# Kernel optimization log

Hardware: AMD Instinct MI355X
Metric: run time of the kernel (lower is better)

The kernel has to match this reference:

```python
import jax, jax.numpy as jnp
import numpy as np

# ViT-B on the Lorentz hyperboloid (curvature C): points x = [x_time, x_space],
# x_time = sqrt(||x_space||^2 + C). All linear/conv/norm ops act on the space
# part and recompute time; residuals/attention-midpoints renormalize the full
# Lorentz vector back onto the hyperboloid.
B, IMG, P, CIN, D, H, L = 32, 224, 16, 3, 768, 12, 12
HD = D // H          # per-head space dim (64)
DFF = 2048           # swiglu hidden: int(2/3 * 4*768) aligned to 64
C = 1.0
EPS = 1e-6


def _time(xs):
    return jnp.sqrt(jnp.clip(jnp.sum(xs * xs, -1, keepdims=True) + C, EPS, None))


def _to_lorentz(xs):
    return jnp.concatenate([_time(xs), xs], -1)


def _project(z):
    # renormalize full Lorentz vector so <z,z>_L = -C
    zz = jnp.sum(z[..., 1:] ** 2, -1, keepdims=True) - z[..., :1] ** 2
    return z * (jnp.sqrt(C) / jnp.sqrt(jnp.clip(-zz, EPS, None)))


def _lorentz_ln(x, g, b):
    xs = x[..., 1:]
    mu = xs.mean(-1, keepdims=True)
    var = ((xs - mu) ** 2).mean(-1, keepdims=True)
    xs = (xs - mu) / jnp.sqrt(var + 1e-6) * g + b
    return _to_lorentz(xs)


def _lresnet(x, y, w):
    # Lorentzian weighted residual: midpoint of x and w*y, projected to manifold
    return _project(x + w * y)


def _rope_tables():
    # 2D axial rope over the 14x14 patch grid, identity rotation for 1 cls token
    n = IMG // P
    d4 = HD // 4
    inv = 1.0 / (100.0 ** (np.arange(d4) / d4))
    ang = np.arange(n)[:, None] * inv[None, :]            # [n, d4]
    ay = np.repeat(ang[:, None, :], n, axis=1)            # row angles
    ax = np.repeat(ang[None, :, :], n, axis=0)            # col angles
    a = np.concatenate([ay, ax], -1).reshape(n * n, HD // 2)
    cos = np.concatenate([np.ones((1, HD // 2)), np.cos(a)], 0)
    sin = np.concatenate([np.zeros((1, HD // 2)), np.sin(a)], 0)
    return jnp.asarray(cos, jnp.float32), jnp.asarray(sin, jnp.float32)


def _apply_rope(x, cos, sin):
    # x: [B,N,H,HD]; rotate consecutive pairs (complex multiply)
    xr = x.reshape(*x.shape[:-1], -1, 2)
    x0, x1 = xr[..., 0], xr[..., 1]
    c = cos[None, :, None, :]
    s = sin[None, :, None, :]
    out = jnp.stack([x0 * c - x1 * s, x0 * s + x1 * c], -1)
    return out.reshape(x.shape)


def _attention(x, Wq, Wk, Wv, Wo, cos, sin, scale):
    b, n, _ = x.shape
    xs = x[..., 1:]
    q = (xs @ Wq).reshape(b, n, H, HD)
    k = (xs @ Wk).reshape(b, n, H, HD)
    v = (xs @ Wv).reshape(b, n, H, HD)
    q = _apply_rope(q, cos, sin)
    k = _apply_rope(k, cos, sin)
    qt = _time(q)[..., 0]   # [B,N,H]
    kt = _time(k)[..., 0]
    # Lorentz inner product <q,k>_L = -q_t k_t + q_s . k_s
    inner = jnp.einsum('bnhd,bmhd->bhnm', q, k) - jnp.einsum('bnh,bmh->bhnm', qt, kt)
    attn = jax.nn.softmax((2.0 * C + 2.0 * inner) / scale, axis=-1)
    vf = jnp.concatenate([_time(v), v], -1)               # [B,M,H,HD+1]
    mid = jnp.einsum('bhnm,bmhe->bnhe', attn, vf)         # Lorentzian midpoint
    mid = _project(mid)
    out_s = mid[..., 1:].reshape(b, n, H * HD) @ Wo       # concat heads + proj
    return _to_lorentz(out_s)


def setup_inputs() -> dict:
    key = jax.random.key(0)
    ks = jax.random.split(key, 12)
    std = 0.02
    nrm = lambda k, shape: jax.random.normal(k, shape, jnp.float32) * std
    return {
        'x': jax.random.normal(ks[0], (B, CIN, IMG, IMG), jnp.float32),
        'cls_s': nrm(ks[1], (D - 1,)),
        'Wp': nrm(ks[2], (P, P, CIN + 1, D - 1)),         # HWIO conv kernel
        'ln1_g': jnp.ones((L, D - 1), jnp.float32),
        'ln1_b': jnp.zeros((L, D - 1), jnp.float32),
        'Wq': nrm(ks[3], (L, D - 1, H * HD)),
        'Wk': nrm(ks[4], (L, D - 1, H * HD)),
        'Wv': nrm(ks[5], (L, D - 1, H * HD)),
        'Wo': nrm(ks[6], (L, H * HD, D - 1)),
        'ln2_g': jnp.ones((L, D - 1), jnp.float32),
        'ln2_b': jnp.zeros((L, D - 1), jnp.float32),
        'W1': nrm(ks[7], (L, D - 1, DFF)),
        'W2': nrm(ks[8], (L, D - 1, DFF)),
        'W3': nrm(ks[9], (L, DFF, D - 1)),
        'wy1': jnp.ones((L,), jnp.float32),
        'wy2': jnp.ones((L,), jnp.float32),
        'lnf_g': jnp.ones((D - 1,), jnp.float32),
        'lnf_b': jnp.zeros((D - 1,), jnp.float32),
    }


def reference(x, cls_s, Wp, ln1_g, ln1_b, Wq, Wk, Wv, Wo, ln2_g, ln2_b,
              W1, W2, W3, wy1, wy2, lnf_g, lnf_b):
    b = x.shape[0]
    xs = jnp.transpose(x, (0, 2, 3, 1))                   # BHWC
    xl = _to_lorentz(xs)                                  # pixel-wise time channel
    feat = jax.lax.conv_general_dilated(
        xl, Wp, (P, P), 'VALID',
        dimension_numbers=('NHWC', 'HWIO', 'NHWC'))       # [B,14,14,D-1]
    tok = _to_lorentz(feat).reshape(b, -1, D)             # [B,196,D]
    cls = jnp.broadcast_to(_to_lorentz(cls_s)[None, None, :], (b, 1, D))
    tok = jnp.concatenate([cls, tok], 1)                  # [B,197,D]
    cos, sin = _rope_tables()
    scale = jnp.sqrt(jnp.asarray(H * HD, jnp.float32))
    for l in range(L):
        xn = _lorentz_ln(tok, ln1_g[l], ln1_b[l])
        a = _attention(xn, Wq[l], Wk[l], Wv[l], Wo[l], cos, sin, scale)
        tok = _lresnet(tok, a, wy1[l])
        xn = _lorentz_ln(tok, ln2_g[l], ln2_b[l])
        hs = xn[..., 1:]
        m = _to_lorentz((jax.nn.silu(hs @ W1[l]) * (hs @ W2[l])) @ W3[l])
        tok = _lresnet(tok, m, wy2[l])
    return _lorentz_ln(tok, lnf_g, lnf_b)
```

## Files before the change

### kernel.cpp

```cpp
#include <hip/hip_runtime.h>
#include <hip/hip_bf16.h>

typedef __attribute__((ext_vector_type(8))) short short8;
typedef __attribute__((ext_vector_type(4))) float f32x4;
typedef _Float16 f16x8 __attribute__((ext_vector_type(8)));

#define NLAYER 12
#define NTOK   6304
#define MPAD   6400
#define CONVM  6272

#define QELE     ((size_t)384*208*64)
#define VELE     ((size_t)384*80*232)

static constexpr size_t AL(size_t x){ return (x + 511) & ~(size_t)511; }
static constexpr size_t B_COS    = 0;
static constexpr size_t B_SIN    = AL(B_COS    + (size_t)197*32*4);
static constexpr size_t B_WPT    = AL(B_SIN    + (size_t)197*32*4);
static constexpr size_t B_APATCH = AL(B_WPT    + (size_t)768*1024*2);
static constexpr size_t B_WQKVT  = AL(B_APATCH + (size_t)CONVM*1024*2);
static constexpr size_t B_WOT    = AL(B_WQKVT  + (size_t)2304*768*2);
static constexpr size_t B_W12T   = AL(B_WOT    + (size_t)768*768*2);
static constexpr size_t B_W3T    = AL(B_W12T   + (size_t)4096*768*2);
static constexpr size_t B_TOK    = AL(B_W3T    + (size_t)768*2048*2);
static constexpr size_t B_ACTA   = AL(B_TOK    + (size_t)NTOK*768*4);
static constexpr size_t B_ACTB   = AL(B_ACTA   + (size_t)MPAD*768*2);
static constexpr size_t B_GOUT   = AL(B_ACTB   + (size_t)MPAD*2048*2);
static constexpr size_t B_QB     = AL(B_GOUT   + (size_t)MPAD*2304*4);
static constexpr size_t B_KB     = AL(B_QB     + QELE*2);
static constexpr size_t B_VT     = AL(B_KB     + QELE*2);
static constexpr size_t B_QTB    = AL(B_VT     + VELE*2);
static constexpr size_t B_KTB    = AL(B_QTB    + (size_t)384*208*4);
static constexpr size_t B_END    = AL(B_KTB    + (size_t)384*208*4);

typedef __attribute__((address_space(1))) unsigned int gu32;
typedef __attribute__((address_space(3))) unsigned int lu32;
__device__ __forceinline__ void gld16(const void* g, void* l) {
  __builtin_amdgcn_global_load_lds((const gu32*)g, (lu32*)l, 16, 0, 0);
}

__device__ __forceinline__ float bsum(float v, float* red) {
  #pragma unroll
  for (int m = 32; m; m >>= 1) v += __shfl_xor(v, m, 64);
  __syncthreads();
  if ((threadIdx.x & 63) == 0) red[threadIdx.x >> 6] = v;
  __syncthreads();
  return red[0] + red[1] + red[2] + red[3];
}

__device__ __forceinline__ ushort h_us(float v) {
  _Float16 h = (_Float16)v;
  return *(ushort*)&h;
}
__device__ __forceinline__ float us_f(ushort u) {
  return (float)*(const _Float16*)&u;
}

__device__ __forceinline__ void xcd_remap(int& bx, int& by) {
  int gx = gridDim.x, gy = gridDim.y;
  int nwg = gx * gy;
  int orig = blockIdx.y * gx + blockIdx.x;
  int q = nwg >> 3, r = nwg & 7;
  int xcd = orig & 7, loc = orig >> 3;
  int wg = (xcd < r ? xcd * (q + 1) : r * (q + 1) + (xcd - r) * q) + loc;
  bx = wg / gy;
  by = wg % gy;
}

__global__ void k_rope_tab(float* __restrict__ cosb, float* __restrict__ sinb) {
  int idx = blockIdx.x * 256 + threadIdx.x;
  if (idx >= 197 * 32) return;
  int p = idx >> 5, j = idx & 31;
  float cv, sv;
  if (p == 0) { cv = 1.f; sv = 0.f; }
  else {
    int pp = p - 1;
    int iy = pp / 14, ix = pp - iy * 14;
    int pos = (j < 16) ? iy : ix;
    int f   = (j < 16) ? j  : j - 16;
    float inv = powf(100.f, -(float)f / 16.f);
    float a = (float)pos * inv;
    cv = cosf(a); sv = sinf(a);
  }
  cosb[idx] = cv; sinb[idx] = sv;
}

__device__ __forceinline__ void tpose_tile(const float* __restrict__ src, ushort* __restrict__ dst,
                                           int K, int N, int ldd, int imode, int tk, int tn) {
  __shared__ float ts[32][33];
  int t = threadIdx.x;
  int rr = t >> 3, c4 = (t & 7) * 4;
  int k0 = tk * 32, n0 = tn * 32;
  #pragma unroll
  for (int e = 0; e < 4; ++e) {
    int k = k0 + rr, n = n0 + c4 + e;
    ts[rr][c4 + e] = (k < K && n < N) ? src[(size_t)k * N + n] : 0.f;
  }
  __syncthreads();
  int c = n0 + rr;
  int drow = (imode == 0) ? c : (16 * (c >> 3) + (c & 7) + (imode == 2 ? 8 : 0));
  ushort4 o;
  #pragma unroll
  for (int e = 0; e < 4; ++e) {
    _Float16 hv = (_Float16)ts[c4 + e][rr];
    ((ushort*)&o)[e] = *(ushort*)&hv;
  }
  *(ushort4*)&dst[(size_t)drow * ldd + k0 + c4] = o;
}

__global__ __launch_bounds__(256) void k_tpose(const float* __restrict__ src, ushort* __restrict__ dst,
                                               int K, int N, int ktiles, int ldd) {
  int tk = blockIdx.x % ktiles, tn = blockIdx.x / ktiles;
  tpose_tile(src, dst, K, N, ldd, 0, tk, tn);
}

__global__ __launch_bounds__(256) void k_wprep(const float* __restrict__ Wq, const float* __restrict__ Wk,
                                               const float* __restrict__ Wv, const float* __restrict__ Wo,
                                               const float* __restrict__ W1, const float* __restrict__ W2,
                                               const float* __restrict__ W3,
                                               ushort* __restrict__ wqkvt, ushort* __restrict__ wot,
                                               ushort* __restrict__ w12t, ushort* __restrict__ w3t) {
  int tile = blockIdx.x;
  const float* src; ushort* dst;
  int K, N, ktiles, ldd, imode = 0, tl;
  if (tile < 2304) {
    int jb = tile / 576; tl = tile % 576;
    ktiles = 24; ldd = 768;
    if (jb == 0)      { src = Wq; dst = wqkvt;                 K = 767; N = 768; }
    else if (jb == 1) { src = Wk; dst = wqkvt + 768 * 768;     K = 767; N = 768; }
    else if (jb == 2) { src = Wv; dst = wqkvt + 2 * 768 * 768; K = 767; N = 768; }
    else              { src = Wo; dst = wot;                   K = 768; N = 767; }
  } else if (tile < 5376) {
    int jb = (tile - 2304) / 1536; tl = (tile - 2304) % 1536;
    ktiles = 24; ldd = 768; K = 767; N = 2048; dst = w12t;
    src = jb ? W2 : W1; imode = jb ? 2 : 1;
  } else {
    tl = tile - 5376; ktiles = 64; ldd = 2048; K = 2048; N = 767; src = W3; dst = w3t;
  }
  int tk = tl % ktiles, tn = tl / ktiles;
  tpose_tile(src, dst, K, N, ldd, imode, tk, tn);
}

__global__ __launch_bounds__(256) void k_im2col(const float* __restrict__ x, ushort* __restrict__ ap) {
  int r = blockIdx.x;
  int b = r / 196, pi = r - b * 196;
  int py = pi / 14, px = pi - py * 14;
  int t = threadIdx.x;
  int ph = t >> 4, pw = t & 15;
  int iy = py * 16 + ph, ix = px * 16 + pw;
  size_t base = ((size_t)b * 3 * 224 + iy) * 224 + ix;
  float x0 = x[base];
  float x1 = x[base + 224 * 224];
  float x2 = x[base + 2 * 224 * 224];
  float tv = sqrtf(fmaxf(x0 * x0 + x1 * x1 + x2 * x2 + 1.f, 1e-6f));
  size_t o = (size_t)r * 1024 + t * 4;
  ap[o] = h_us(tv); ap[o + 1] = h_us(x0); ap[o + 2] = h_us(x1); ap[o + 3] = h_us(x2);
}

template<int MODE>
__global__ __launch_bounds__(256) void k_gemmh(const ushort* __restrict__ A, const ushort* __restrict__ Bt,
                                               float* __restrict__ C, ushort* __restrict__ H,
                                               int N, int K) {
  __shared__ ushort sA[128 * 64];
  __shared__ ushort sB[128 * 64];
  int bx, by;
  xcd_remap(bx, by);
  int m0 = bx * 128, n0 = by * 128;
  int t = threadIdx.x;
  int w = t >> 6, l = t & 63;
  int wm = (w >> 1) * 64, wn = (w & 1) * 64;
  int lr = l & 15, hi = l >> 4;
  f32x4 acc[4][4] = {};
  for (int k0 = 0; k0 < K; k0 += 64) {
    #pragma unroll
    for (int i = 0; i < 4; ++i) {
      int fl = i * 256 + t;
      int r = fl >> 3, c = fl & 7;
      int cs = c ^ (r & 7);
      gld16(&A[(size_t)(m0 + r) * K + k0 + cs * 8], &sA[fl * 8]);
      gld16(&Bt[(size_t)(n0 + r) * K + k0 + cs * 8], &sB[fl * 8]);
    }
    __syncthreads();
    f16x8 af[4][2], bfr[4][2];
    #pragma unroll
    for (int q = 0; q < 4; ++q) {
      int ra = wm + q * 16 + lr, rb = wn + q * 16 + lr;
      #pragma unroll
      for (int h = 0; h < 2; ++h) {
        af[q][h]  = *(const f16x8*)&sA[ra * 64 + ((h * 4 + hi) ^ (ra & 7)) * 8];
        bfr[q][h] = *(const f16x8*)&sB[rb * 64 + ((h * 4 + hi) ^ (rb & 7)) * 8];
      }
    }
    #pragma unroll
    for (int mi = 0; mi < 4; ++mi)
      #pragma unroll
      for (int ni = 0; ni < 4; ++ni) {
        acc[mi][ni] = __builtin_amdgcn_mfma_f32_16x16x32_f16(af[mi][0], bfr[ni][0], acc[mi][ni], 0, 0, 0);
        acc[mi][ni] = __builtin_amdgcn_mfma_f32_16x16x32_f16(af[mi][1], bfr[ni][1], acc[mi][ni], 0, 0, 0);
      }
    __syncthreads();
  }
  int rr = hi * 4, cc = lr;
  if (MODE == 1) {
    #pragma unroll
    for (int mi = 0; mi < 4; ++mi)
      #pragma unroll
      for (int ni = 0; ni < 4; ++ni) {
        int g = (n0 + wn + ni * 16) >> 4;
        #pragma unroll
        for (int j = 0; j < 4; ++j) {
          float v = acc[mi][ni][j];
          float p = __shfl_xor(v, 8);
          float u1 = (cc < 8) ? v : p;
          float u2 = (cc < 8) ? p : v;
          float hv = u1 / (1.f + __expf(-u1)) * u2;
          if (cc < 8)
            H[(size_t)(m0 + wm + mi * 16 + rr + j) * 2048 + g * 8 + cc] = h_us(hv);
        }
      }
  } else if (MODE == 3) {
    #pragma unroll
    for (int mi = 0; mi < 4; ++mi)
      #pragma unroll
      for (int ni = 0; ni < 4; ++ni)
        #pragma unroll
        for (int j = 0; j < 4; ++j)
          H[(size_t)(m0 + wm + mi * 16 + rr + j) * N + (n0 + wn + ni * 16 + cc)] = h_us(acc[mi][ni][j]);
  } else {
    #pragma unroll
    for (int mi = 0; mi < 4; ++mi)
      #pragma unroll
      for (int ni = 0; ni < 4; ++ni)
        #pragma unroll
        for (int j = 0; j < 4; ++j)
          C[(size_t)(m0 + wm + mi * 16 + rr + j) * N + (n0 + wn + ni * 16 + cc)] = acc[mi][ni][j];
  }
}

template<int MODE>
__global__ __launch_bounds__(512, 2) void k_g256(const ushort* __restrict__ A, const ushort* __restrict__ Bt,
                                                 ushort* __restrict__ H, int N, int K,
                                                 ushort* __restrict__ qbuf, ushort* __restrict__ kbuf,
                                                 ushort* __restrict__ vtb,
                                                 float* __restrict__ qtb, float* __restrict__ ktb,
                                                 const float* __restrict__ cosb, const float* __restrict__ sinb) {
  __shared__ ushort sA[2][2][256 * 32];
  __shared__ ushort sB[2][2][256 * 32];
  const int t = threadIdx.x;
  const int w = t >> 6, l = t & 63;
  const int wr = w >> 2, wc = w & 3;
  const int lr = l & 15, hi4 = l >> 4;
  int bx, by;
  xcd_remap(bx, by);
  const int m0 = bx * 256, n0 = by * 256;

  auto stageA = [&](int kt, int kh, int buf) {
    #pragma unroll
    for (int ii = 0; ii < 2; ++ii) {
      int q = ii * 512 + t;
      int r = q >> 2, ci = q & 3;
      gld16(&A[(size_t)(m0 + r) * K + kt * 64 + kh * 32 + ((ci ^ ((r >> 1) & 3)) * 8)], &sA[buf][kh][q * 8]);
    }
  };
  auto stageB = [&](int kt, int kh, int buf) {
    #pragma unroll
    for (int ii = 0; ii < 2; ++ii) {
      int q = ii * 512 + t;
      int r = q >> 2, ci = q & 3;
      gld16(&Bt[(size_t)(n0 + r) * K + kt * 64 + kh * 32 + ((ci ^ ((r >> 1) & 3)) * 8)], &sB[buf][kh][q * 8]);
    }
  };

  f32x4 acc[8][4] = {};
  auto ldA = [&](int buf, int ks, int G, f16x8* fr) {
    #pragma unroll
    for (int mi = 0; mi < 4; ++mi) {
      int r = wr * 128 + (G * 4 + mi) * 16 + lr;
      fr[mi] = *(const f16x8*)&sA[buf][ks][(r * 4 + (hi4 ^ ((r >> 1) & 3))) * 8];
    }
  };
  auto ldB = [&](int buf, int ks, f16x8* fr) {
    #pragma unroll
    for (int ni = 0; ni < 4; ++ni) {
      int r = wc * 64 + ni * 16 + lr;
      fr[ni] = *(const f16x8*)&sB[buf][ks][(r * 4 + (hi4 ^ ((r >> 1) & 3))) * 8];
    }
  };
  auto mmaG = [&](int G, f16x8* a, f16x8* b) {
    __builtin_amdgcn_s_setprio(1);
    #pragma unroll
    for (int mi = 0; mi < 4; ++mi)
      #pragma unroll
      for (int ni = 0; ni < 4; ++ni)
        acc[G * 4 + mi][ni] = __builtin_amdgcn_mfma_f32_16x16x32_f16(a[mi], b[ni], acc[G * 4 + mi][ni], 0, 0, 0);
    __builtin_amdgcn_s_setprio(0);
  };

  const int NT = K >> 6;
  const int NI = NT >> 1;
  stageA(0, 0, 0); stageB(0, 0, 0); stageA(0, 1, 0); stageB(0, 1, 0);

  for (int i = 0; i < NI; ++i) {
    const int T1 = 2 * i + 1, T2 = 2 * i + 2;
    const bool last = (i == NI - 1);
    f16x8 a0[4], a1[4], b0[4], b1[4];
    asm volatile("s_waitcnt vmcnt(4)" ::: "memory");
    __builtin_amdgcn_sched_barrier(0);
    __builtin_amdgcn_s_barrier();
    ldA(0, 0, 0, a0); ldB(0, 0, b0);
    stageA(T1, 0, 1);
    mmaG(0, a0, b0);
    ldA(0, 0, 1, a1);
    stageB(T1, 0, 1);
    mmaG(1, a1, b0);
    asm volatile("s_waitcnt vmcnt(4)" ::: "memory");
    __builtin_amdgcn_sched_barrier(0);
    __builtin_amdgcn_s_barrier();
    ldA(0, 1, 0, a0); ldB(0, 1, b1);
    stageA(T1, 1, 1);
    mmaG(0, a0, b1);
    ldA(0, 1, 1, a1);
    stageB(T1, 1, 1);
    mmaG(1, a1, b1);
    asm volatile("s_waitcnt vmcnt(4)" ::: "memory");
    __builtin_amdgcn_sched_barrier(0);
    __builtin_amdgcn_s_barrier();
    ldA(1, 0, 0, a0); ldB(1, 0, b0);
    if (!last) stageA(T2, 0, 0);
    mmaG(0, a0, b0);
    ldA(1, 0, 1, a1);
    if (!last) stageB(T2, 0, 0);
    mmaG(1, a1, b0);
    if (last) { asm volatile("s_waitcnt vmcnt(0)" ::: "memory"); }
    else      { asm volatile("s_waitcnt vmcnt(4)" ::: "memory"); }
    __builtin_amdgcn_sched_barrier(0);
    __builtin_amdgcn_s_barrier();
    ldA(1, 1, 0, a0); ldB(1, 1, b1);
    if (!last) stageA(T2, 1, 0);
    mmaG(0, a0, b1);
    ldA(1, 1, 1, a1);
    if (!last) stageB(T2, 1, 0);
    mmaG(1, a1, b1);
  }

  if (MODE == 2) {
    int secBase = n0 + wc * 64;
    int sec = secBase / 768;
    int hh = (secBase - sec * 768) >> 6;
    #pragma unroll
    for (int mi = 0; mi < 8; ++mi) {
      float nrm[4];
      #pragma unroll
      for (int j = 0; j < 4; ++j) {
        float ss = 0.f;
        #pragma unroll
        for (int ni = 0; ni < 4; ++ni) ss += acc[mi][ni][j] * acc[mi][ni][j];
        #pragma unroll
        for (int m = 8; m; m >>= 1) ss += __shfl_xor(ss, m, 64);
        nrm[j] = sqrtf(fmaxf(ss + 1.f, 1e-6f));
      }
      #pragma unroll
      for (int j = 0; j < 4; ++j) {
        int m = m0 + wr * 128 + mi * 16 + hi4 * 4 + j;
        if (m < NTOK) {
          int b = m / 197, nn = m - b * 197;
          int bh = b * 12 + hh;
          if (sec == 2) {
            size_t vo = (size_t)bh * 80 * 232;
            if (lr == 0) vtb[vo + nn] = h_us(nrm[j]);
            #pragma unroll
            for (int ni = 0; ni < 4; ++ni) {
              int e = ni * 16 + lr;
              vtb[vo + (size_t)(1 + e) * 232 + nn] = h_us(acc[mi][ni][j]);
            }
          } else {
            float* tb = (sec == 0) ? qtb : ktb;
            ushort* ob = (sec == 0) ? qbuf : kbuf;
            if (lr == 0) tb[(size_t)bh * 208 + nn] = nrm[j];
            size_t rowb = ((size_t)bh * 208 + nn) * 64;
            #pragma unroll
            for (int ni = 0; ni < 4; ++ni) {
              int d = ni * 16 + lr;
              float v = acc[mi][ni][j];
              float p = __shfl_xor(v, 1);
              int j2 = d >> 1;
              float cz = cosb[nn * 32 + j2], sz = sinb[nn * 32 + j2];
              float rv = ((lr & 1) == 0) ? (v * cz - p * sz) : (p * sz + v * cz);
              ob[rowb + d] = h_us(rv);
            }
          }
        }
      }
    }
  }
}

__global__ __launch_bounds__(256) void k_build_tok(const float* __restrict__ feat, const float* __restrict__ cls,
                                                   float* __restrict__ tok) {
  __shared__ float red[8];
  int r = blockIdx.x;
  int b = r / 197, i = r - b * 197;
  int t = threadIdx.x;
  const float* src = (i == 0) ? cls : (feat + (size_t)(b * 196 + i - 1) * 768);
  float v0 = src[t], v1 = src[256 + t], v2 = (t < 255) ? src[512 + t] : 0.f;
  float qs = bsum(v0 * v0 + v1 * v1 + v2 * v2, red);
  float* tp = tok + (size_t)r * 768;
  if (t == 0) tp[0] = sqrtf(fmaxf(qs + 1.f, 1e-6f));
  tp[1 + t] = v0; tp[257 + t] = v1; if (t < 255) tp[513 + t] = v2;
}

__global__ __launch_bounds__(256) void k_ln(const float* __restrict__ tok, const float* __restrict__ g,
                                            const float* __restrict__ bb, ushort* __restrict__ out) {
  __shared__ float red[8];
  int r = blockIdx.x, t = threadIdx.x;
  const float* xp = tok + (size_t)r * 768;
  float v0 = xp[1 + t], v1 = xp[257 + t], v2 = (t < 255) ? xp[513 + t] : 0.f;
  float s = bsum(v0 + v1 + v2, red);
  float q = bsum(v0 * v0 + v1 * v1 + v2 * v2, red);
  float mu = s * (1.f / 767.f);
  float rstd = rsqrtf(fmaxf(q * (1.f / 767.f) - mu * mu, 0.f) + 1e-6f);
  size_t o = (size_t)r * 768;
  out[o + t]       = h_us((v0 - mu) * rstd * g[t]       + bb[t]);
  out[o + 256 + t] = h_us((v1 - mu) * rstd * g[256 + t] + bb[256 + t]);
  if (t < 255)
    out[o + 512 + t] = h_us((v2 - mu) * rstd * g[512 + t] + bb[512 + t]);
  if (t == 255) out[o + 767] = 0;
}

__global__ __launch_bounds__(128) void k_attn(const ushort* __restrict__ qbuf,
                                              const float* __restrict__ qtb,
                                              const ushort* __restrict__ kbuf,
                                              const float* __restrict__ ktb,
                                              const ushort* __restrict__ vtb,
                                              ushort* __restrict__ outa) {
  __shared__ ushort sP[2][16 * 248];
  int bxt = blockIdx.x, bh = blockIdx.y;
  int b = bh / 12, hd = bh - b * 12;
  int t = threadIdx.x, w = t >> 6, l = t & 63;
  int rt = bxt * 2 + w;
  if (rt >= 13) return;
  int lr = l & 15, hi4 = l >> 4;
  const ushort* qg = qbuf + (size_t)bh * 208 * 64;
  const ushort* kg = kbuf + (size_t)bh * 208 * 64;
  const ushort* vg = vtb + (size_t)bh * 80 * 232;
  const float*  ktp = ktb + (size_t)bh * 208;
  const float invs = 0.03608439182435161f;
  ushort* pw = &sP[w][0];

  int qrow = (rt * 16 + lr) * 64 + hi4 * 8;
  f16x8 q0 = *(const f16x8*)&qg[qrow];
  f16x8 q1 = *(const f16x8*)&qg[qrow + 32];
  float qt4[4];
  #pragma unroll
  for (int j = 0; j < 4; ++j) qt4[j] = qtb[(size_t)bh * 208 + rt * 16 + hi4 * 4 + j];
  f32x4 acc[13];
  #pragma unroll
  for (int nt = 0; nt < 13; ++nt) {
    int kr = (nt * 16 + lr) * 64 + hi4 * 8;
    f16x8 k0 = *(const f16x8*)&kg[kr];
    f16x8 k1 = *(const f16x8*)&kg[kr + 32];
    acc[nt] = (f32x4){0.f, 0.f, 0.f, 0.f};
    acc[nt] = __builtin_amdgcn_mfma_f32_16x16x32_f16(q0, k0, acc[nt], 0, 0, 0);
    acc[nt] = __builtin_amdgcn_mfma_f32_16x16x32_f16(q1, k1, acc[nt], 0, 0, 0);
  }
  float mx[4] = {-1e30f, -1e30f, -1e30f, -1e30f};
  #pragma unroll
  for (int nt = 0; nt < 13; ++nt) {
    int cI = nt * 16 + lr;
    float ktc = ktp[cI];
    bool valid = (cI < 197);
    #pragma unroll
    for (int j = 0; j < 4; ++j) {
      float s = (2.f + 2.f * (acc[nt][j] - qt4[j] * ktc)) * invs;
      acc[nt][j] = s;
      if (valid) mx[j] = fmaxf(mx[j], s);
    }
  }
  #pragma unroll
  for (int j = 0; j < 4; ++j)
    #pragma unroll
    for (int m = 8; m; m >>= 1) mx[j] = fmaxf(mx[j], __shfl_xor(mx[j], m, 64));
  #pragma unroll
  for (int nt = 0; nt < 14; ++nt) {
    int cI = nt * 16 + lr;
    #pragma unroll
    for (int j = 0; j < 4; ++j) {
      float p = (nt < 13 && cI < 197) ? __expf(acc[nt][j] - mx[j]) : 0.f;
      pw[(hi4 * 4 + j) * 248 + cI] = h_us(p);
    }
  }
  f32x4 accO[5];
  #pragma unroll
  for (int et = 0; et < 5; ++et) accO[et] = (f32x4){0.f, 0.f, 0.f, 0.f};
  #pragma unroll
  for (int ks = 0; ks < 7; ++ks) {
    f16x8 pa = *(const f16x8*)&pw[lr * 248 + ks * 32 + hi4 * 8];
    #pragma unroll
    for (int et = 0; et < 5; ++et) {
      int er = et * 16 + lr;
      f16x8 bv = *(const f16x8*)&vg[(er > 64 ? 64 : er) * 232 + ks * 32 + hi4 * 8];
      accO[et] = __builtin_amdgcn_mfma_f32_16x16x32_f16(pa, bv, accO[et], 0, 0, 0);
    }
  }
  float ssq[4] = {0.f, 0.f, 0.f, 0.f};
  #pragma unroll
  for (int et = 0; et < 4; ++et)
    #pragma unroll
    for (int j = 0; j < 4; ++j) ssq[j] += accO[et][j] * accO[et][j];
  if (lr == 0) {
    #pragma unroll
    for (int j = 0; j < 4; ++j) ssq[j] += accO[4][j] * accO[4][j];
  }
  #pragma unroll
  for (int j = 0; j < 4; ++j)
    #pragma unroll
    for (int m = 8; m; m >>= 1) ssq[j] += __shfl_xor(ssq[j], m, 64);
  float rf4[4];
  #pragma unroll
  for (int j = 0; j < 4; ++j) {
    float o0 = __shfl(accO[0][j], (l & 48));
    rf4[j] = rsqrtf(fmaxf(2.f * o0 * o0 - ssq[j], 1e-6f));
  }
  #pragma unroll
  for (int et = 0; et < 5; ++et) {
    int e = et * 16 + lr;
    if (e == 0 || e >= 65) continue;
    #pragma unroll
    for (int j = 0; j < 4; ++j) {
      int n = rt * 16 + hi4 * 4 + j;
      if (n < 197)
        outa[((size_t)(b * 197 + n)) * 768 + hd * 64 + (e - 1)] = h_us(accO[et][j] * rf4[j]);
    }
  }
}

template<int FIN>
__global__ __launch_bounds__(256) void k_resnet_ln(float* __restrict__ tok, const ushort* __restrict__ s,
                                                   const float* __restrict__ wyp, int l,
                                                   const float* __restrict__ g, const float* __restrict__ bb,
                                                   ushort* __restrict__ out16, float* __restrict__ out32) {
  __shared__ float red[8];
  __shared__ float bc[1];
  int r = blockIdx.x, t = threadIdx.x;
  float w = wyp[l];
  const ushort* sp = s + (size_t)r * 768;
  float* tp = tok + (size_t)r * 768;
  float s0 = us_f(sp[t]), s1 = us_f(sp[256 + t]), s2 = (t < 255) ? us_f(sp[512 + t]) : 0.f;
  float qs = bsum(s0 * s0 + s1 * s1 + s2 * s2, red);
  float at = sqrtf(fmaxf(qs + 1.f, 1e-6f));
  float z0 = tp[1 + t] + w * s0;
  float z1 = tp[257 + t] + w * s1;
  float z2 = (t < 255) ? (tp[513 + t] + w * s2) : 0.f;
  float zs = bsum(z0 * z0 + z1 * z1 + z2 * z2, red);
  if (t == 0) bc[0] = tp[0] + w * at;
  __syncthreads();
  float zt = bc[0];
  float rf = rsqrtf(fmaxf(zt * zt - zs, 1e-6f));
  float n0 = z0 * rf, n1 = z1 * rf, n2 = z2 * rf;
  tp[1 + t] = n0; tp[257 + t] = n1; if (t < 255) tp[513 + t] = n2;
  if (t == 0) tp[0] = zt * rf;
  float sm = bsum(n0 + n1 + n2, red);
  float sq = bsum(n0 * n0 + n1 * n1 + n2 * n2, red);
  float mu = sm * (1.f / 767.f);
  float rstd = rsqrtf(fmaxf(sq * (1.f / 767.f) - mu * mu, 0.f) + 1e-6f);
  float y0 = (n0 - mu) * rstd * g[t] + bb[t];
  float y1 = (n1 - mu) * rstd * g[256 + t] + bb[256 + t];
  float y2 = (t < 255) ? ((n2 - mu) * rstd * g[512 + t] + bb[512 + t]) : 0.f;
  if (FIN) {
    float qq = bsum(y0 * y0 + y1 * y1 + y2 * y2, red);
    float* op = out32 + (size_t)r * 768;
    op[1 + t] = y0; op[257 + t] = y1; if (t < 255) op[513 + t] = y2;
    if (t == 0) op[0] = sqrtf(fmaxf(qq + 1.f, 1e-6f));
  } else {
    size_t o = (size_t)r * 768;
    out16[o + t] = h_us(y0);
    out16[o + 256 + t] = h_us(y1);
    if (t < 255) out16[o + 512 + t] = h_us(y2);
    if (t == 255) out16[o + 767] = 0;
  }
}

extern "C" void kernel_launch(void* const* d_in, const int* in_sizes, int n_in,
                              void* d_out, int out_size, void* d_ws, size_t ws_size,
                              hipStream_t stream) {
  const float* x     = (const float*)d_in[0];
  const float* cls_s = (const float*)d_in[1];
  const float* Wp    = (const float*)d_in[2];
  const float* ln1g  = (const float*)d_in[3];
  const float* ln1b  = (const float*)d_in[4];
  const float* Wq    = (const float*)d_in[5];
  const float* Wk    = (const float*)d_in[6];
  const float* Wv    = (const float*)d_in[7];
  const float* Wo    = (const float*)d_in[8];
  const float* ln2g  = (const float*)d_in[9];
  const float* ln2b  = (const float*)d_in[10];
  const float* W1    = (const float*)d_in[11];
  const float* W2    = (const float*)d_in[12];
  const float* W3    = (const float*)d_in[13];
  const float* wy1   = (const float*)d_in[14];
  const float* wy2   = (const float*)d_in[15];
  const float* lnfg  = (const float*)d_in[16];
  const float* lnfb  = (const float*)d_in[17];

  if (ws_size < B_END) return;

  char* ws = (char*)d_ws;
  float*  cosb   = (float*)(ws + B_COS);
  float*  sinb   = (float*)(ws + B_SIN);
  ushort* wpt    = (ushort*)(ws + B_WPT);
  ushort* apatch = (ushort*)(ws + B_APATCH);
  ushort* wqkvt  = (ushort*)(ws + B_WQKVT);
  ushort* wot    = (ushort*)(ws + B_WOT);
  ushort* w12t   = (ushort*)(ws + B_W12T);
  ushort* w3t    = (ushort*)(ws + B_W3T);
  float*  tok    = (float*)(ws + B_TOK);
  ushort* acta   = (ushort*)(ws + B_ACTA);
  ushort* actb   = (ushort*)(ws + B_ACTB);
  float*  gout   = (float*)(ws + B_GOUT);
  ushort* gouth  = (ushort*)(ws + B_GOUT);
  ushort* qbuf   = (ushort*)(ws + B_QB);
  ushort* kbuf   = (ushort*)(ws + B_KB);
  ushort* vtb    = (ushort*)(ws + B_VT);
  float*  qtb    = (float*)(ws + B_QTB);
  float*  ktb    = (float*)(ws + B_KTB);

  hipMemsetAsync(vtb, 0, VELE * 2, stream);

  k_rope_tab<<<25, 256, 0, stream>>>(cosb, sinb);
  k_tpose<<<32 * 24, 256, 0, stream>>>(Wp, wpt, 1024, 767, 32, 1024);
  k_im2col<<<CONVM, 256, 0, stream>>>(x, apatch);
  k_gemmh<0><<<dim3(49, 6), 256, 0, stream>>>(apatch, wpt, gout, nullptr, 768, 1024);
  k_build_tok<<<NTOK, 256, 0, stream>>>(gout, cls_s, tok);
  k_ln<<<NTOK, 256, 0, stream>>>(tok, ln1g, ln1b, acta);

  for (int l = 0; l < NLAYER; ++l) {
    k_wprep<<<6912, 256, 0, stream>>>(Wq + (size_t)l * 767 * 768, Wk + (size_t)l * 767 * 768,
                                      Wv + (size_t)l * 767 * 768, Wo + (size_t)l * 768 * 767,
                                      W1 + (size_t)l * 767 * 2048, W2 + (size_t)l * 767 * 2048,
                                      W3 + (size_t)l * 2048 * 767, wqkvt, wot, w12t, w3t);

    k_g256<2><<<dim3(25, 9), 512, 0, stream>>>(acta, wqkvt, nullptr, 2304, 768,
                                               qbuf, kbuf, vtb, qtb, ktb, cosb, sinb);
    k_attn<<<dim3(7, 384), 128, 0, stream>>>(qbuf, qtb, kbuf, ktb, vtb, acta);
    k_gemmh<3><<<dim3(50, 6), 256, 0, stream>>>(acta, wot, nullptr, gouth, 768, 768);
    k_resnet_ln<0><<<NTOK, 256, 0, stream>>>(tok, gouth, wy1, l,
                                             ln2g + (size_t)l * 767, ln2b + (size_t)l * 767, acta, nullptr);

    k_gemmh<1><<<dim3(50, 32), 256, 0, stream>>>(acta, w12t, nullptr, actb, 4096, 768);
    k_gemmh<3><<<dim3(50, 6), 256, 0, stream>>>(actb, w3t, nullptr, gouth, 768, 2048);
    if (l < NLAYER - 1)
      k_resnet_ln<0><<<NTOK, 256, 0, stream>>>(tok, gouth, wy2, l,
                                               ln1g + (size_t)(l + 1) * 767, ln1b + (size_t)(l + 1) * 767,
                                               acta, nullptr);
    else
      k_resnet_ln<1><<<NTOK, 256, 0, stream>>>(tok, gouth, wy2, l, lnfg, lnfb, nullptr, (float*)d_out);
  }
}
```

Baseline: 3.156 ms.

## Batch all-layer weight prep into one launch and double-buffer GEMM LDS tiles

Weight transposition and f16 conversion for all twelve layers now runs in a single kernel launch up front instead of one launch per layer, with per-layer weight buffers in workspace. This removes twelve serialized small launches from the critical path at the cost of more workspace memory. The k_gemmh kernel now uses two LDS buffers and issues the next k-tile's global-to-LDS loads before computing on the current tile, so load latency can overlap with MFMA work. That doubles shared memory per block, which may lower occupancy. The GOUT buffer is also shrunk.

Result: slower. 3.263 ms (+3.4%).

```diff
diff --git a/kernel.cpp b/kernel.cpp
--- a/kernel.cpp
+++ b/kernel.cpp
@@ -12,6 +12,11 @@
 
 #define QELE     ((size_t)384*208*64)
 #define VELE     ((size_t)384*80*232)
+
+#define WS_QKV ((size_t)2304*768)
+#define WS_WO  ((size_t)768*768)
+#define WS_W12 ((size_t)4096*768)
+#define WS_W3  ((size_t)768*2048)
 
 static constexpr size_t AL(size_t x){ return (x + 511) & ~(size_t)511; }
 static constexpr size_t B_COS    = 0;
@@ -19,14 +24,14 @@
 static constexpr size_t B_WPT    = AL(B_SIN    + (size_t)197*32*4);
 static constexpr size_t B_APATCH = AL(B_WPT    + (size_t)768*1024*2);
 static constexpr size_t B_WQKVT  = AL(B_APATCH + (size_t)CONVM*1024*2);
-static constexpr size_t B_WOT    = AL(B_WQKVT  + (size_t)2304*768*2);
-static constexpr size_t B_W12T   = AL(B_WOT    + (size_t)768*768*2);
-static constexpr size_t B_W3T    = AL(B_W12T   + (size_t)4096*768*2);
-static constexpr size_t B_TOK    = AL(B_W3T    + (size_t)768*2048*2);
+static constexpr size_t B_WOT    = AL(B_WQKVT  + WS_QKV*NLAYER*2);
+static constexpr size_t B_W12T   = AL(B_WOT    + WS_WO*NLAYER*2);
+static constexpr size_t B_W3T    = AL(B_W12T   + WS_W12*NLAYER*2);
+static constexpr size_t B_TOK    = AL(B_W3T    + WS_W3*NLAYER*2);
 static constexpr size_t B_ACTA   = AL(B_TOK    + (size_t)NTOK*768*4);
 static constexpr size_t B_ACTB   = AL(B_ACTA   + (size_t)MPAD*768*2);
 static constexpr size_t B_GOUT   = AL(B_ACTB   + (size_t)MPAD*2048*2);
-static constexpr size_t B_QB     = AL(B_GOUT   + (size_t)MPAD*2304*4);
+static constexpr size_t B_QB     = AL(B_GOUT   + (size_t)MPAD*768*4);
 static constexpr size_t B_KB     = AL(B_QB     + QELE*2);
 static constexpr size_t B_VT     = AL(B_KB     + QELE*2);
 static constexpr size_t B_QTB    = AL(B_VT     + VELE*2);
@@ -114,28 +119,41 @@
   tpose_tile(src, dst, K, N, ldd, 0, tk, tn);
 }
 
-__global__ __launch_bounds__(256) void k_wprep(const float* __restrict__ Wq, const float* __restrict__ Wk,
-                                               const float* __restrict__ Wv, const float* __restrict__ Wo,
-                                               const float* __restrict__ W1, const float* __restrict__ W2,
-                                               const float* __restrict__ W3,
-                                               ushort* __restrict__ wqkvt, ushort* __restrict__ wot,
-                                               ushort* __restrict__ w12t, ushort* __restrict__ w3t) {
-  int tile = blockIdx.x;
+__global__ __launch_bounds__(256) void k_wprep12(const float* __restrict__ Wq, const float* __restrict__ Wk,
+                                                 const float* __restrict__ Wv, const float* __restrict__ Wo,
+                                                 const float* __restrict__ W1, const float* __restrict__ W2,
+                                                 const float* __restrict__ W3,
+                                                 ushort* __restrict__ wqkvt, ushort* __restrict__ wot,
+                                                 ushort* __restrict__ w12t, ushort* __restrict__ w3t) {
+  int gt = blockIdx.x;
+  int l = gt / 6912;
+  int tile = gt - l * 6912;
+  const float* q  = Wq + (size_t)l * 767 * 768;
+  const float* kk = Wk + (size_t)l * 767 * 768;
+  const float* v  = Wv + (size_t)l * 767 * 768;
+  const float* o  = Wo + (size_t)l * 768 * 767;
+  const float* w1 = W1 + (size_t)l * 767 * 2048;
+  const float* w2 = W2 + (size_t)l * 767 * 2048;
+  const float* w3 = W3 + (size_t)l * 2048 * 767;
+  ushort* dqkv = wqkvt + (size_t)l * WS_QKV;
+  ushort* dwo  = wot   + (size_t)l * WS_WO;
+  ushort* dw12 = w12t  + (size_t)l * WS_W12;
+  ushort* dw3  = w3t   + (size_t)l * WS_W3;
   const float* src; ushort* dst;
   int K, N, ktiles, ldd, imode = 0, tl;
   if (tile < 2304) {
     int jb = tile / 576; tl = tile % 576;
     ktiles = 24; ldd = 768;
-    if (jb == 0)      { src = Wq; dst = wqkvt;                 K = 767; N = 768; }
-    else if (jb == 1) { src = Wk; dst = wqkvt + 768 * 768;     K = 767; N = 768; }
-    else if (jb == 2) { src = Wv; dst = wqkvt + 2 * 768 * 768; K = 767; N = 768; }
-    else              { src = Wo; dst = wot;                   K = 768; N = 767; }
+    if (jb == 0)      { src = q;  dst = dqkv;                 K = 767; N = 768; }
+    else if (jb == 1) { src = kk; dst = dqkv + 768 * 768;     K = 767; N = 768; }
+    else if (jb == 2) { src = v;  dst = dqkv + 2 * 768 * 768; K = 767; N = 768; }
+    else              { src = o;  dst = dwo;                  K = 768; N = 767; }
   } else if (tile < 5376) {
     int jb = (tile - 2304) / 1536; tl = (tile - 2304) % 1536;
-    ktiles = 24; ldd = 768; K = 767; N = 2048; dst = w12t;
-    src = jb ? W2 : W1; imode = jb ? 2 : 1;
+    ktiles = 24; ldd = 768; K = 767; N = 2048; dst = dw12;
+    src = jb ? w2 : w1; imode = jb ? 2 : 1;
   } else {
-    tl = tile - 5376; ktiles = 64; ldd = 2048; K = 2048; N = 767; src = W3; dst = w3t;
+    tl = tile - 5376; ktiles = 64; ldd = 2048; K = 2048; N = 767; src = w3; dst = dw3;
   }
   int tk = tl % ktiles, tn = tl / ktiles;
   tpose_tile(src, dst, K, N, ldd, imode, tk, tn);
@@ -161,8 +179,8 @@
 __global__ __launch_bounds__(256) void k_gemmh(const ushort* __restrict__ A, const ushort* __restrict__ Bt,
                                                float* __restrict__ C, ushort* __restrict__ H,
                                                int N, int K) {
-  __shared__ ushort sA[128 * 64];
-  __shared__ ushort sB[128 * 64];
+  __shared__ ushort sA[2][128 * 64];
+  __shared__ ushort sB[2][128 * 64];
   int bx, by;
   xcd_remap(bx, by);
   int m0 = bx * 128, n0 = by * 128;
@@ -170,25 +188,32 @@
   int w = t >> 6, l = t & 63;
   int wm = (w >> 1) * 64, wn = (w & 1) * 64;
   int lr = l & 15, hi = l >> 4;
-  f32x4 acc[4][4] = {};
-  for (int k0 = 0; k0 < K; k0 += 64) {
+
+  auto stage = [&](int k0, int buf) {
     #pragma unroll
     for (int i = 0; i < 4; ++i) {
       int fl = i * 256 + t;
       int r = fl >> 3, c = fl & 7;
       int cs = c ^ (r & 7);
-      gld16(&A[(size_t)(m0 + r) * K + k0 + cs * 8], &sA[fl * 8]);
-      gld16(&Bt[(size_t)(n0 + r) * K + k0 + cs * 8], &sB[fl * 8]);
-    }
-    __syncthreads();
+      gld16(&A[(size_t)(m0 + r) * K + k0 + cs * 8], &sA[buf][fl * 8]);
+      gld16(&Bt[(size_t)(n0 + r) * K + k0 + cs * 8], &sB[buf][fl * 8]);
+    }
+  };
+
+  f32x4 acc[4][4] = {};
+  stage(0, 0);
+  __syncthreads();
+  int buf = 0;
+  for (int k0 = 0; k0 < K; k0 += 64) {
+    if (k0 + 64 < K) stage(k0 + 64, buf ^ 1);
     f16x8 af[4][2], bfr[4][2];
     #pragma unroll
     for (int q = 0; q < 4; ++q) {
       int ra = wm + q * 16 + lr, rb = wn + q * 16 + lr;
       #pragma unroll
       for (int h = 0; h < 2; ++h) {
-        af[q][h]  = *(const f16x8*)&sA[ra * 64 + ((h * 4 + hi) ^ (ra & 7)) * 8];
-        bfr[q][h] = *(const f16x8*)&sB[rb * 64 + ((h * 4 + hi) ^ (rb & 7)) * 8];
+        af[q][h]  = *(const f16x8*)&sA[buf][ra * 64 + ((h * 4 + hi) ^ (ra & 7)) * 8];
+        bfr[q][h] = *(const f16x8*)&sB[buf][rb * 64 + ((h * 4 + hi) ^ (rb & 7)) * 8];
       }
     }
     #pragma unroll
@@ -199,7 +224,9 @@
         acc[mi][ni] = __builtin_amdgcn_mfma_f32_16x16x32_f16(af[mi][1], bfr[ni][1], acc[mi][ni], 0, 0, 0);
       }
     __syncthreads();
-  }
+    buf ^= 1;
+  }
+
   int rr = hi * 4, cc = lr;
   if (MODE == 1) {
     #pragma unroll
@@ -629,25 +656,26 @@
   k_rope_tab<<<25, 256, 0, stream>>>(cosb, sinb);
   k_tpose<<<32 * 24, 256, 0, stream>>>(Wp, wpt, 1024, 767, 32, 1024);
   k_im2col<<<CONVM, 256, 0, stream>>>(x, apatch);
+  k_wprep12<<<6912 * NLAYER, 256, 0, stream>>>(Wq, Wk, Wv, Wo, W1, W2, W3, wqkvt, wot, w12t, w3t);
   k_gemmh<0><<<dim3(49, 6), 256, 0, stream>>>(apatch, wpt, gout, nullptr, 768, 1024);
   k_build_tok<<<NTOK, 256, 0, stream>>>(gout, cls_s, tok);
   k_ln<<<NTOK, 256, 0, stream>>>(tok, ln1g, ln1b, acta);
 
   for (int l = 0; l < NLAYER; ++l) {
-    k_wprep<<<6912, 256, 0, stream>>>(Wq + (size_t)l * 767 * 768, Wk + (size_t)l * 767 * 768,
-                                      Wv + (size_t)l * 767 * 768, Wo + (size_t)l * 768 * 767,
-                                      W1 + (size_t)l * 767 * 2048, W2 + (size_t)l * 767 * 2048,
-                                      W3 + (size_t)l * 2048 * 767, wqkvt, wot, w12t, w3t);
-
-    k_g256<2><<<dim3(25, 9), 512, 0, stream>>>(acta, wqkvt, nullptr, 2304, 768,
+    const ushort* wq_l  = wqkvt + (size_t)l * WS_QKV;
+    const ushort* wo_l  = wot   + (size_t)l * WS_WO;
+    const ushort* w12_l = w12t  + (size_t)l * WS_W12;
+    const ushort* w3_l  = w3t   + (size_t)l * WS_W3;
+
+    k_g256<2><<<dim3(25, 9), 512, 0, stream>>>(acta, wq_l, nullptr, 2304, 768,
                                                qbuf, kbuf, vtb, qtb, ktb, cosb, sinb);
     k_attn<<<dim3(7, 384), 128, 0, stream>>>(qbuf, qtb, kbuf, ktb, vtb, acta);
-    k_gemmh<3><<<dim3(50, 6), 256, 0, stream>>>(acta, wot, nullptr, gouth, 768, 768);
+    k_gemmh<3><<<dim3(50, 6), 256, 0, stream>>>(acta, wo_l, nullptr, gouth, 768, 768);
     k_resnet_ln<0><<<NTOK, 256, 0, stream>>>(tok, gouth, wy1, l,
                                              ln2g + (size_t)l * 767, ln2b + (size_t)l * 767, acta, nullptr);
 
-    k_gemmh<1><<<dim3(50, 32), 256, 0, stream>>>(acta, w12t, nullptr, actb, 4096, 768);
-    k_gemmh<3><<<dim3(50, 6), 256, 0, stream>>>(actb, w3t, nullptr, gouth, 768, 2048);
+    k_gemmh<1><<<dim3(50, 32), 256, 0, stream>>>(acta, w12_l, nullptr, actb, 4096, 768);
+    k_gemmh<3><<<dim3(50, 6), 256, 0, stream>>>(actb, w3_l, nullptr, gouth, 768, 2048);
     if (l < NLAYER - 1)
       k_resnet_ln<0><<<NTOK, 256, 0, stream>>>(tok, gouth, wy2, l,
                                                ln1g + (size_t)(l + 1) * 767, ln1b + (size_t)(l + 1) * 767,
```
